# Optimization experiments

Measured on AMD Instinct MI355X. Metric: run time of the kernel, lower is better.

## Reference

```python
import jax, jax.numpy as jnp
import numpy as np

N_NODES = 100000
N_EDGES = 1200000
D = 64


def setup_inputs() -> dict:
    key = jax.random.key(0)
    k1, k2, k3, k4, k5 = jax.random.split(key, 5)
    node_feat = jax.random.normal(k1, (N_NODES, D), dtype=jnp.float32)
    edge_feat = jax.random.normal(k2, (N_EDGES, D), dtype=jnp.float32)
    edge_index = jax.random.randint(k3, (2, N_EDGES), 0, N_NODES, dtype=jnp.int32)
    # torch.nn.Linear default init ~ U(-1/sqrt(fan_in), 1/sqrt(fan_in)); scaled normals are fine for a reference
    W1 = jax.random.normal(k4, (D, 2 * D), dtype=jnp.float32) / np.sqrt(D)
    b1 = jnp.zeros((2 * D,), dtype=jnp.float32)
    W2 = jax.random.normal(k5, (2 * D, D), dtype=jnp.float32) / np.sqrt(2 * D)
    b2 = jnp.zeros((D,), dtype=jnp.float32)
    return {"node_feat": node_feat, "edge_feat": edge_feat, "edge_index": edge_index,
            "W1": W1, "b1": b1, "W2": W2, "b2": b2}


def reference(node_feat, edge_feat, edge_index, W1, b1, W2, b2):
    src, dst = edge_index[0], edge_index[1]
    # send: message on each edge = src node feature + edge feature  [E, D]
    msg = node_feat[src] + edge_feat
    # recv: sum-reduce messages into destination nodes  [N, D]
    agg = jax.ops.segment_sum(msg, dst, num_segments=node_feat.shape[0])
    # 2-layer MLP: Linear(D, 2D) -> ReLU -> Linear(2D, D)
    h = jax.nn.relu(agg @ W1 + b1)
    out = h @ W2 + b2
    return out
```

## Files before the change

### kernel.cpp

```cpp
#include <hip/hip_runtime.h>

#define N_NODES 100000
#define N_EDGES 1200000
#define D 64
#define D2 128
#define NPB 32
#define NG (N_NODES / NPB)
#define SCAN_BLK 256
#define N_SCAN_BLKS ((N_NODES + SCAN_BLK - 1) / SCAN_BLK)
#define CNT_PAD 100352
#define BKT_LDS 512

typedef float f4v __attribute__((ext_vector_type(4)));
typedef int   i2v __attribute__((ext_vector_type(2)));

__device__ __forceinline__ float4 ldnt4(const float* p) {
    f4v v = __builtin_nontemporal_load((const f4v*)p);
    return make_float4(v.x, v.y, v.z, v.w);
}
__device__ __forceinline__ void stnt4(float* p, float4 v) {
    f4v t = {v.x, v.y, v.z, v.w};
    __builtin_nontemporal_store(t, (f4v*)p);
}
__device__ __forceinline__ int2 ldnt_i2(const int2* p) {
    i2v v = __builtin_nontemporal_load((const i2v*)p);
    return make_int2(v.x, v.y);
}
__device__ __forceinline__ void stnt_i2(int2* p, int2 v) {
    i2v t = {v.x, v.y};
    __builtin_nontemporal_store(t, (i2v*)p);
}


__global__ __launch_bounds__(256) void hist_kernel(
    const int* __restrict__ dst, int* __restrict__ counts) {
    int e = blockIdx.x * 256 + threadIdx.x;
    if (e < N_EDGES) {
        int d = __builtin_nontemporal_load(dst + e);
        atomicAdd(&counts[d], 1);
    }
}

__global__ __launch_bounds__(SCAN_BLK) void scan1_kernel(
    const int* __restrict__ counts, int* __restrict__ offsets,
    int* __restrict__ partials) {
    __shared__ int s[2][SCAN_BLK];
    int t = threadIdx.x, i = blockIdx.x * SCAN_BLK + t;
    int c = (i < N_NODES) ? counts[i] : 0;
    int pin = 0;
    s[0][t] = c; __syncthreads();
    for (int off = 1; off < SCAN_BLK; off <<= 1) {
        int v = s[pin][t] + ((t >= off) ? s[pin][t - off] : 0);
        s[pin ^ 1][t] = v; pin ^= 1; __syncthreads();
    }
    int incl = s[pin][t];
    if (i < N_NODES) offsets[i] = incl - c;
    if (t == SCAN_BLK - 1) partials[blockIdx.x] = incl;
}

__global__ __launch_bounds__(512) void scan2_kernel(
    const int* __restrict__ partials, int* __restrict__ scanned) {
    __shared__ int s[2][512];
    int t = threadIdx.x;
    int c = (t < N_SCAN_BLKS) ? partials[t] : 0;
    int pin = 0;
    s[0][t] = c; __syncthreads();
    for (int off = 1; off < 512; off <<= 1) {
        int v = s[pin][t] + ((t >= off) ? s[pin][t - off] : 0);
        s[pin ^ 1][t] = v; pin ^= 1; __syncthreads();
    }
    if (t < N_SCAN_BLKS) scanned[t] = s[pin][t] - c;
}

__global__ __launch_bounds__(SCAN_BLK) void scan3_kernel(
    int* __restrict__ offsets, int* __restrict__ cursors,
    const int* __restrict__ scanned) {
    int i = blockIdx.x * SCAN_BLK + threadIdx.x;
    if (i < N_NODES) {
        int o = offsets[i] + scanned[blockIdx.x];
        offsets[i] = o;
        cursors[i] = o;
        if (i == N_NODES - 1) offsets[N_NODES] = N_EDGES;
    }
}

__global__ __launch_bounds__(256) void bucket_kernel(
    const int* __restrict__ src, const int* __restrict__ dst,
    int* __restrict__ cursors, int2* __restrict__ buckets) {
    int e = blockIdx.x * 256 + threadIdx.x;
    if (e < N_EDGES) {
        int s = __builtin_nontemporal_load(src + e);
        int d = __builtin_nontemporal_load(dst + e);
        int pos = atomicAdd(&cursors[d], 1);
        stnt_i2(&buckets[pos], make_int2(s, e));
    }
}

__device__ __forceinline__ void fma4(float4& acc, float s, const float4& w) {
    acc.x = fmaf(s, w.x, acc.x); acc.y = fmaf(s, w.y, acc.y);
    acc.z = fmaf(s, w.z, acc.z); acc.w = fmaf(s, w.w, acc.w);
}

__global__ __launch_bounds__(256) void gather_mlp_kernel(
    const float* __restrict__ nf, const float* __restrict__ ef,
    const int* __restrict__ offsets, const int2* __restrict__ buckets,
    const float* __restrict__ W1, const float* __restrict__ b1,
    const float* __restrict__ W2, const float* __restrict__ b2,
    float* __restrict__ out) {
    __shared__ float s_agg[NPB][D + 4];
    __shared__ float s_h[NPB][D2 + 4];
    __shared__ int s_off[NPB + 1];
    int2* s_bkt = (int2*)&s_h[0][0];

    const int tid = threadIdx.x;
    const int lane = tid & 63;
    const int wv = tid >> 6;
    const int base = blockIdx.x * NPB;

    const int goff = offsets[base];
    const int bcnt = offsets[base + NPB] - goff;
    const int scnt = min(bcnt, BKT_LDS);

    if (tid <= NPB) s_off[tid] = offsets[base + tid];
    for (int i = tid; i < scnt; i += 256) s_bkt[i] = ldnt_i2(&buckets[goff + i]);
    __syncthreads();

    const int sub = lane >> 4;
    const int c4 = (lane & 15) << 2;

    for (int r = 0; r < 8; r++) {
        const int slot = wv * 8 + r;
        const int abs0 = s_off[slot];
        const int cnt = s_off[slot + 1] - abs0;
        const int loc0 = abs0 - goff;
        float4 accA = make_float4(0.f, 0.f, 0.f, 0.f);
        float4 accB = make_float4(0.f, 0.f, 0.f, 0.f);
        for (int i = 0; i < cnt; i += 8) {
            int j0 = i + sub, j1 = i + 4 + sub;
            if (j0 < cnt) {
                int lj = loc0 + j0;
                int2 p = (lj < scnt) ? s_bkt[lj] : buckets[abs0 + j0];
                float4 a = *(const float4*)(nf + (p.x << 6) + c4);
                float4 b = ldnt4(ef + ((long long)p.y << 6) + c4);
                accA.x += a.x + b.x; accA.y += a.y + b.y;
                accA.z += a.z + b.z; accA.w += a.w + b.w;
            }
            if (j1 < cnt) {
                int lj = loc0 + j1;
                int2 p = (lj < scnt) ? s_bkt[lj] : buckets[abs0 + j1];
                float4 a = *(const float4*)(nf + (p.x << 6) + c4);
                float4 b = ldnt4(ef + ((long long)p.y << 6) + c4);
                accB.x += a.x + b.x; accB.y += a.y + b.y;
                accB.z += a.z + b.z; accB.w += a.w + b.w;
            }
        }
        accA.x += accB.x; accA.y += accB.y; accA.z += accB.z; accA.w += accB.w;
        accA.x += __shfl_xor(accA.x, 16); accA.y += __shfl_xor(accA.y, 16);
        accA.z += __shfl_xor(accA.z, 16); accA.w += __shfl_xor(accA.w, 16);
        accA.x += __shfl_xor(accA.x, 32); accA.y += __shfl_xor(accA.y, 32);
        accA.z += __shfl_xor(accA.z, 32); accA.w += __shfl_xor(accA.w, 32);
        if (sub == 0) *(float4*)&s_agg[slot][c4] = accA;
    }
    __syncthreads();

    {
        const int jg = tid & 31, ng = tid >> 5;
        const int j0 = jg * 4, n0 = ng * 4;
        float4 bb = *(const float4*)(b1 + j0);
        float4 acc0 = bb, acc1 = bb, acc2 = bb, acc3 = bb;
        for (int d = 0; d < D; d += 4) {
            float4 a0 = *(const float4*)&s_agg[n0 + 0][d];
            float4 a1 = *(const float4*)&s_agg[n0 + 1][d];
            float4 a2 = *(const float4*)&s_agg[n0 + 2][d];
            float4 a3 = *(const float4*)&s_agg[n0 + 3][d];
            float4 w0 = *(const float4*)(W1 + (d + 0) * D2 + j0);
            float4 w1 = *(const float4*)(W1 + (d + 1) * D2 + j0);
            float4 w2 = *(const float4*)(W1 + (d + 2) * D2 + j0);
            float4 w3 = *(const float4*)(W1 + (d + 3) * D2 + j0);
            fma4(acc0, a0.x, w0); fma4(acc0, a0.y, w1); fma4(acc0, a0.z, w2); fma4(acc0, a0.w, w3);
            fma4(acc1, a1.x, w0); fma4(acc1, a1.y, w1); fma4(acc1, a1.z, w2); fma4(acc1, a1.w, w3);
            fma4(acc2, a2.x, w0); fma4(acc2, a2.y, w1); fma4(acc2, a2.z, w2); fma4(acc2, a2.w, w3);
            fma4(acc3, a3.x, w0); fma4(acc3, a3.y, w1); fma4(acc3, a3.z, w2); fma4(acc3, a3.w, w3);
        }
        *(float4*)&s_h[n0 + 0][j0] = make_float4(fmaxf(acc0.x,0.f), fmaxf(acc0.y,0.f), fmaxf(acc0.z,0.f), fmaxf(acc0.w,0.f));
        *(float4*)&s_h[n0 + 1][j0] = make_float4(fmaxf(acc1.x,0.f), fmaxf(acc1.y,0.f), fmaxf(acc1.z,0.f), fmaxf(acc1.w,0.f));
        *(float4*)&s_h[n0 + 2][j0] = make_float4(fmaxf(acc2.x,0.f), fmaxf(acc2.y,0.f), fmaxf(acc2.z,0.f), fmaxf(acc2.w,0.f));
        *(float4*)&s_h[n0 + 3][j0] = make_float4(fmaxf(acc3.x,0.f), fmaxf(acc3.y,0.f), fmaxf(acc3.z,0.f), fmaxf(acc3.w,0.f));
    }
    __syncthreads();

    {
        const int kg = tid & 15, ng = tid >> 4;
        const int k0 = kg * 4, n0 = ng * 2;
        float4 bb = *(const float4*)(b2 + k0);
        float4 o0 = bb, o1 = bb;
        for (int j = 0; j < D2; j += 4) {
            float4 h0 = *(const float4*)&s_h[n0 + 0][j];
            float4 h1 = *(const float4*)&s_h[n0 + 1][j];
            float4 w0 = *(const float4*)(W2 + (j + 0) * D + k0);
            float4 w1 = *(const float4*)(W2 + (j + 1) * D + k0);
            float4 w2 = *(const float4*)(W2 + (j + 2) * D + k0);
            float4 w3 = *(const float4*)(W2 + (j + 3) * D + k0);
            fma4(o0, h0.x, w0); fma4(o0, h0.y, w1); fma4(o0, h0.z, w2); fma4(o0, h0.w, w3);
            fma4(o1, h1.x, w0); fma4(o1, h1.y, w1); fma4(o1, h1.z, w2); fma4(o1, h1.w, w3);
        }
        long long na = (long long)base + n0;
        stnt4(out + na * D + k0, o0);
        stnt4(out + (na + 1) * D + k0, o1);
    }
}

extern "C" void kernel_launch(void* const* d_in, const int* in_sizes, int n_in,
                              void* d_out, int out_size, void* d_ws, size_t ws_size,
                              hipStream_t stream) {
    const float* node_feat = (const float*)d_in[0];
    const float* edge_feat = (const float*)d_in[1];
    const int*   edge_index = (const int*)d_in[2];
    const float* W1 = (const float*)d_in[3];
    const float* b1 = (const float*)d_in[4];
    const float* W2 = (const float*)d_in[5];
    const float* b2 = (const float*)d_in[6];
    float* out = (float*)d_out;

    const int* src = edge_index;
    const int* dst = edge_index + N_EDGES;

    int* counts   = (int*)d_ws;
    int* offsets  = counts + CNT_PAD;
    int* cursors  = counts + 2 * CNT_PAD;
    int* partials = counts + 3 * CNT_PAD;
    int* scanned  = partials + 512;
    int2* buckets = (int2*)(scanned + 512);

    hipMemsetAsync(counts, 0, CNT_PAD * sizeof(int), stream);

    const int eblocks = (N_EDGES + 255) / 256;
    hist_kernel<<<eblocks, 256, 0, stream>>>(dst, counts);
    scan1_kernel<<<N_SCAN_BLKS, SCAN_BLK, 0, stream>>>(counts, offsets, partials);
    scan2_kernel<<<1, 512, 0, stream>>>(partials, scanned);
    scan3_kernel<<<N_SCAN_BLKS, SCAN_BLK, 0, stream>>>(offsets, cursors, scanned);
    bucket_kernel<<<eblocks, 256, 0, stream>>>(src, dst, cursors, buckets);

    gather_mlp_kernel<<<NG, 256, 0, stream>>>(
        node_feat, edge_feat, offsets, buckets, W1, b1, W2, b2, out);
}
```

Measured before the change: 676.8 us.

## Balance edge gather across wavefront sub-groups using LDS atomics and row lookup table

The per-node gather loop, where each wavefront handled 8 fixed node slots, is replaced by an edge-balanced split. The block's edge range is divided evenly among 16 sub-groups, each edge's destination row comes from a precomputed LDS byte lookup table built by binary search, and results are accumulated with LDS float atomics using staggered component order. The bucket LDS capacity is raised to 768 entries. This removes load imbalance from skewed in-degrees, at the cost of LDS atomic contention, an extra sync and lookup-table build, and non-deterministic summation order.

```diff
diff --git a/kernel.cpp b/kernel.cpp
--- a/kernel.cpp
+++ b/kernel.cpp
@@ -9,7 +9,7 @@
 #define SCAN_BLK 256
 #define N_SCAN_BLKS ((N_NODES + SCAN_BLK - 1) / SCAN_BLK)
 #define CNT_PAD 100352
-#define BKT_LDS 512
+#define BKT_LDS 768
 
 typedef float f4v __attribute__((ext_vector_type(4)));
 typedef int   i2v __attribute__((ext_vector_type(2)));
@@ -101,6 +101,12 @@
     acc.z = fmaf(s, w.z, acc.z); acc.w = fmaf(s, w.w, acc.w);
 }
 
+__device__ __forceinline__ int bsearch_row(const int* s_off, int key) {
+    int lo = 0, hi = NPB;
+    while (hi - lo > 1) { int mid = (lo + hi) >> 1; if (s_off[mid] <= key) lo = mid; else hi = mid; }
+    return lo;
+}
+
 __global__ __launch_bounds__(256) void gather_mlp_kernel(
     const float* __restrict__ nf, const float* __restrict__ ef,
     const int* __restrict__ offsets, const int2* __restrict__ buckets,
@@ -111,6 +117,7 @@
     __shared__ float s_h[NPB][D2 + 4];
     __shared__ int s_off[NPB + 1];
     int2* s_bkt = (int2*)&s_h[0][0];
+    unsigned char* s_lut = (unsigned char*)(s_bkt + BKT_LDS);
 
     const int tid = threadIdx.x;
     const int lane = tid & 63;
@@ -122,44 +129,35 @@
     const int scnt = min(bcnt, BKT_LDS);
 
     if (tid <= NPB) s_off[tid] = offsets[base + tid];
+    for (int i = tid; i < NPB * (D + 4); i += 256) ((float*)s_agg)[i] = 0.f;
     for (int i = tid; i < scnt; i += 256) s_bkt[i] = ldnt_i2(&buckets[goff + i]);
     __syncthreads();
 
-    const int sub = lane >> 4;
-    const int c4 = (lane & 15) << 2;
-
-    for (int r = 0; r < 8; r++) {
-        const int slot = wv * 8 + r;
-        const int abs0 = s_off[slot];
-        const int cnt = s_off[slot + 1] - abs0;
-        const int loc0 = abs0 - goff;
-        float4 accA = make_float4(0.f, 0.f, 0.f, 0.f);
-        float4 accB = make_float4(0.f, 0.f, 0.f, 0.f);
-        for (int i = 0; i < cnt; i += 8) {
-            int j0 = i + sub, j1 = i + 4 + sub;
-            if (j0 < cnt) {
-                int lj = loc0 + j0;
-                int2 p = (lj < scnt) ? s_bkt[lj] : buckets[abs0 + j0];
-                float4 a = *(const float4*)(nf + (p.x << 6) + c4);
-                float4 b = ldnt4(ef + ((long long)p.y << 6) + c4);
-                accA.x += a.x + b.x; accA.y += a.y + b.y;
-                accA.z += a.z + b.z; accA.w += a.w + b.w;
-            }
-            if (j1 < cnt) {
-                int lj = loc0 + j1;
-                int2 p = (lj < scnt) ? s_bkt[lj] : buckets[abs0 + j1];
-                float4 a = *(const float4*)(nf + (p.x << 6) + c4);
-                float4 b = ldnt4(ef + ((long long)p.y << 6) + c4);
-                accB.x += a.x + b.x; accB.y += a.y + b.y;
-                accB.z += a.z + b.z; accB.w += a.w + b.w;
+    for (int e = tid; e < scnt; e += 256) s_lut[e] = (unsigned char)bsearch_row(s_off, goff + e);
+    __syncthreads();
+
+    {
+        const int sub = lane >> 4;
+        const int c4 = (lane & 15) << 2;
+        const int sid = wv * 4 + sub;
+        const int slen = (bcnt + 15) >> 4;
+        const int e0 = sid * slen;
+        const int e1 = min(e0 + slen, bcnt);
+        const int st = (lane >> 2) & 3;
+        #pragma unroll 2
+        for (int e = e0; e < e1; ++e) {
+            int2 p; int r;
+            if (e < scnt) { p = s_bkt[e]; r = (int)s_lut[e]; }
+            else          { p = ldnt_i2(&buckets[goff + e]); r = bsearch_row(s_off, goff + e); }
+            float4 a = *(const float4*)(nf + (p.x << 6) + c4);
+            float4 b = ldnt4(ef + ((long long)p.y << 6) + c4);
+            float v[4] = {a.x + b.x, a.y + b.y, a.z + b.z, a.w + b.w};
+            #pragma unroll
+            for (int k = 0; k < 4; ++k) {
+                int kk = (k + st) & 3;
+                atomicAdd(&s_agg[r][c4 + kk], v[kk]);
             }
         }
-        accA.x += accB.x; accA.y += accB.y; accA.z += accB.z; accA.w += accB.w;
-        accA.x += __shfl_xor(accA.x, 16); accA.y += __shfl_xor(accA.y, 16);
-        accA.z += __shfl_xor(accA.z, 16); accA.w += __shfl_xor(accA.w, 16);
-        accA.x += __shfl_xor(accA.x, 32); accA.y += __shfl_xor(accA.y, 32);
-        accA.z += __shfl_xor(accA.z, 32); accA.w += __shfl_xor(accA.w, 32);
-        if (sub == 0) *(float4*)&s_agg[slot][c4] = accA;
     }
     __syncthreads();
 
```

Measured after the change: 943.7 us. 1.39x slower.
